# Optimization experiments

Hardware: AMD Instinct MI355X
Metric: run time of the kernel (lower is better)

## Reference

```python
import math
import jax, jax.numpy as jnp
import numpy as np

W_BITS = 8
A_BITS = 8
N_HEADS = 16

def fake_quant(x, bits):
    # symmetric per-tensor fake quantization with straight-through estimator
    if bits >= 32:
        return x
    qmax = float(2 ** (bits - 1) - 1)
    scale = jnp.maximum(jnp.max(jnp.abs(x)) / qmax, 1e-8)
    q = jnp.round(x / scale) * scale
    return x + jax.lax.stop_gradient(q - x)

def qlinear(x, W, b):
    # QuantizeLinear: quantize activations (a_bits) and weights (w_bits), then y = x @ W^T + b
    xq = fake_quant(x, A_BITS)
    Wq = fake_quant(W, W_BITS)
    return jnp.einsum('bsd,ed->bse', xq, Wq) + b

def setup_inputs() -> dict:
    key = jax.random.key(0)
    B, S, D = 2, 2048, 1024
    ks = jax.random.split(key, 6)
    inp = {
        'hidden_states': jax.random.normal(ks[0], (B, S, D), dtype=jnp.float32),
        'attention_mask': jnp.ones((B, S), dtype=jnp.float32),
        'Wq': 0.02 * jax.random.normal(ks[1], (D, D), dtype=jnp.float32),
        'bq': jnp.zeros((D,), dtype=jnp.float32),
        'Wk': 0.02 * jax.random.normal(ks[2], (D, D), dtype=jnp.float32),
        'bk': jnp.zeros((D,), dtype=jnp.float32),
        'Wv': 0.02 * jax.random.normal(ks[3], (D, D), dtype=jnp.float32),
        'bv': jnp.zeros((D,), dtype=jnp.float32),
        'Wo': 0.02 * jax.random.normal(ks[4], (D, D), dtype=jnp.float32),
        'bo': jnp.zeros((D,), dtype=jnp.float32),
    }
    return inp

def reference(hidden_states, attention_mask, Wq, bq, Wk, bk, Wv, bv, Wo, bo):
    B, S, D = hidden_states.shape
    H = N_HEADS
    hd = D // H

    q = qlinear(hidden_states, Wq, bq).reshape(B, S, H, hd)
    k = qlinear(hidden_states, Wk, bk).reshape(B, S, H, hd)
    v = qlinear(hidden_states, Wv, bv).reshape(B, S, H, hd)

    # scores: [B, H, Sq, Sk]
    scores = jnp.einsum('bqhd,bkhd->bhqk', q, k) / math.sqrt(hd)
    mask_bias = (1.0 - attention_mask)[:, None, None, :] * -10000.0
    scores = scores + mask_bias
    probs = jax.nn.softmax(scores, axis=-1)

    attn = jnp.einsum('bhqk,bkhd->bqhd', probs, v).reshape(B, S, D)
    return qlinear(attn, Wo, bo)
```

## Files before the change

kernel.cpp:

```cpp
#include <hip/hip_runtime.h>
#include <cstddef>
#include <cstdint>

constexpr int Bb = 2, Ss = 2048, Dd = 1024, Hh = 16, HD = 64;
constexpr int Mm = Bb * Ss;

typedef int v4i __attribute__((ext_vector_type(4)));
typedef __bf16 bf16x8 __attribute__((ext_vector_type(8)));
typedef __bf16 bf16x2 __attribute__((ext_vector_type(2)));
typedef float f32x16 __attribute__((ext_vector_type(16)));

#define QPOSTMUL 0.18033688f
#define MASKBIAS -14426.950408f

__device__ __forceinline__ float qscale(float amax) {
    return fmaxf(amax / 127.0f, 1e-8f);
}

__device__ __forceinline__ unsigned short bf16rtn(float x) {
    __bf16 b = (__bf16)x;
    return __builtin_bit_cast(unsigned short, b);
}

__device__ __forceinline__ unsigned pack_bf16x2(float a, float b) {
    bf16x2 h;
    h[0] = (__bf16)a;
    h[1] = (__bf16)b;
    return __builtin_bit_cast(unsigned, h);
}

__global__ void amax_all(const float4* __restrict__ hidden,
                         const float4* __restrict__ w0, const float4* __restrict__ w1,
                         const float4* __restrict__ w2, const float4* __restrict__ w3,
                         unsigned* __restrict__ slots) {
    const float4* src; int n4, slot, bx, nb;
    if (blockIdx.x < 448) { src = hidden; n4 = Mm * Dd / 4; slot = 0; bx = blockIdx.x; nb = 448; }
    else {
        int w = (blockIdx.x - 448) >> 4; bx = (blockIdx.x - 448) & 15; nb = 16;
        src = w == 0 ? w0 : w == 1 ? w1 : w == 2 ? w2 : w3;
        n4 = Dd * Dd / 4; slot = 1 + w;
    }
    float m = 0.f;
    for (int i = bx * blockDim.x + threadIdx.x; i < n4; i += nb * blockDim.x) {
        float4 v = src[i];
        m = fmaxf(m, fmaxf(fmaxf(fabsf(v.x), fabsf(v.y)), fmaxf(fabsf(v.z), fabsf(v.w))));
    }
    #pragma unroll
    for (int off = 32; off > 0; off >>= 1) m = fmaxf(m, __shfl_down(m, off, 64));
    __shared__ float sm[4];
    int lane = threadIdx.x & 63, wid = threadIdx.x >> 6;
    if (lane == 0) sm[wid] = m;
    __syncthreads();
    if (threadIdx.x == 0) {
        float mm = fmaxf(fmaxf(sm[0], sm[1]), fmaxf(sm[2], sm[3]));
        atomicMax(slots + slot, __float_as_uint(mm));
    }
}

__global__ void quant_all(const float* __restrict__ hidden,
                          const float* __restrict__ w0, const float* __restrict__ w1,
                          const float* __restrict__ w2, const float* __restrict__ w3,
                          const float* __restrict__ amax,
                          char* __restrict__ hq8, char* __restrict__ Wall8) {
    const float* x; char* y; int n4, slot, bx, nb;
    if (blockIdx.x < 1024) { x = hidden; y = hq8; n4 = Mm * Dd / 4; slot = 0; bx = blockIdx.x; nb = 1024; }
    else {
        int w = (blockIdx.x - 1024) >> 5; bx = (blockIdx.x - 1024) & 31; nb = 32;
        x = w == 0 ? w0 : w == 1 ? w1 : w == 2 ? w2 : w3;
        y = Wall8 + ((size_t)w << 20);
        n4 = Dd * Dd / 4; slot = 1 + w;
    }
    float s = qscale(amax[slot]);
    const float4* x4 = (const float4*)x;
    char4* y4 = (char4*)y;
    for (int i = bx * blockDim.x + threadIdx.x; i < n4; i += nb * blockDim.x) {
        float4 v = x4[i];
        char4 q;
        q.x = (char)(int)rintf(v.x / s);
        q.y = (char)(int)rintf(v.y / s);
        q.z = (char)(int)rintf(v.z / s);
        q.w = (char)(int)rintf(v.w / s);
        y4[i] = q;
    }
}

__global__ void quant_a(const float* __restrict__ x, char* __restrict__ y,
                        const float* __restrict__ amax, int n4) {
    float s = qscale(amax[0]);
    int stride = gridDim.x * blockDim.x;
    const float4* x4 = (const float4*)x;
    char4* y4 = (char4*)y;
    for (int i = blockIdx.x * blockDim.x + threadIdx.x; i < n4; i += stride) {
        float4 v = x4[i];
        char4 q;
        q.x = (char)(int)rintf(v.x / s);
        q.y = (char)(int)rintf(v.y / s);
        q.z = (char)(int)rintf(v.z / s);
        q.w = (char)(int)rintf(v.w / s);
        y4[i] = q;
    }
}

#define GLOAD_LDS16(g, l) __builtin_amdgcn_global_load_lds( \
    (const __attribute__((address_space(1))) unsigned int*)(g), \
    (__attribute__((address_space(3))) unsigned int*)(l), 16, 0, 0)

__device__ __forceinline__ void gemm128_core(const char* __restrict__ A, const char* __restrict__ Bw,
                                             int bm, int bn, int K, int t,
                                             char* At, char* Bt, v4i acc[4][4]) {
    const int lane = t & 63, w = t >> 6;
    const int wm = (w >> 1) * 64, wn = (w & 1) * 64;
    const int lr = lane & 15, kq = lane >> 4;
    const int rs = w * 16 + (lane >> 2);
    const int cc = lane & 3;

    for (int k0 = 0; k0 < K; k0 += 64) {
        __syncthreads();
        #pragma unroll
        for (int h = 0; h < 2; h++) {
            int r = rs + h * 64;
            int cs = cc ^ ((r >> 1) & 3);
            GLOAD_LDS16(A  + (size_t)(bm + r) * K + k0 + cs * 16, At + r * 64 + cc * 16);
            GLOAD_LDS16(Bw + (size_t)(bn + r) * K + k0 + cs * 16, Bt + r * 64 + cc * 16);
        }
        __syncthreads();

        v4i af[4], bf[4];
        #pragma unroll
        for (int mt = 0; mt < 4; mt++) {
            int row = wm + mt * 16 + lr;
            af[mt] = *(const v4i*)(At + row * 64 + ((kq ^ ((row >> 1) & 3)) << 4));
        }
        #pragma unroll
        for (int nt = 0; nt < 4; nt++) {
            int row = wn + nt * 16 + lr;
            bf[nt] = *(const v4i*)(Bt + row * 64 + ((kq ^ ((row >> 1) & 3)) << 4));
        }
        #pragma unroll
        for (int mt = 0; mt < 4; mt++)
            #pragma unroll
            for (int nt = 0; nt < 4; nt++)
                acc[mt][nt] = __builtin_amdgcn_mfma_i32_16x16x64_i8(af[mt], bf[nt], acc[mt][nt], 0, 0, 0);
    }
}

__global__ __launch_bounds__(256) void gemm_qkv(const char* __restrict__ A,
                                                const char* __restrict__ Wall8,
                                                const float* __restrict__ bq,
                                                const float* __restrict__ bk,
                                                const float* __restrict__ bv,
                                                const float* __restrict__ amax,
                                                unsigned short* __restrict__ qb16,
                                                unsigned short* __restrict__ kb16,
                                                unsigned short* __restrict__ vt16) {
    __shared__ alignas(16) char pool[34816];
    char* At = pool;
    char* Bt = pool + 8192;
    unsigned short (*Tt)[136] = (unsigned short(*)[136])pool;

    const int t = threadIdx.x, lane = t & 63, w = t >> 6;
    const int mat = blockIdx.x >> 3;
    const int bn = (blockIdx.x & 7) * 128, bm = blockIdx.y * 128;
    const int wm = (w >> 1) * 64, wn = (w & 1) * 64;
    const int lr = lane & 15, kq = lane >> 4;

    const v4i vzero = {0, 0, 0, 0};
    v4i acc[4][4];
    #pragma unroll
    for (int mt = 0; mt < 4; mt++)
        #pragma unroll
        for (int nt = 0; nt < 4; nt++) acc[mt][nt] = vzero;

    const char* Bw = Wall8 + ((size_t)mat << 20);
    gemm128_core(A, Bw, bm, bn, Dd, t, At, Bt, acc);

    const float* bias = mat == 0 ? bq : mat == 1 ? bk : bv;
    float sc = qscale(amax[0]) * qscale(amax[1 + mat]);
    float pm = (mat == 0) ? QPOSTMUL : 1.0f;

    __syncthreads();

    if (mat != 2) {
        #pragma unroll
        for (int nt = 0; nt < 4; nt++) {
            int n_l = wn + nt * 16 + lr;
            float bv_ = bias[bn + n_l];
            #pragma unroll
            for (int mt = 0; mt < 4; mt++) {
                int m_l = wm + mt * 16 + kq * 4;
                #pragma unroll
                for (int rg = 0; rg < 4; rg++)
                    Tt[m_l + rg][n_l] = bf16rtn(((float)acc[mt][nt][rg] * sc + bv_) * pm);
            }
        }
    } else {
        #pragma unroll
        for (int nt = 0; nt < 4; nt++) {
            int n_l = wn + nt * 16 + lr;
            float bv_ = bias[bn + n_l];
            #pragma unroll
            for (int mt = 0; mt < 4; mt++) {
                int m_l = wm + mt * 16 + kq * 4;
                ushort4 hv;
                hv.x = bf16rtn((float)acc[mt][nt][0] * sc + bv_);
                hv.y = bf16rtn((float)acc[mt][nt][1] * sc + bv_);
                hv.z = bf16rtn((float)acc[mt][nt][2] * sc + bv_);
                hv.w = bf16rtn((float)acc[mt][nt][3] * sc + bv_);
                *(ushort4*)&Tt[n_l][m_l] = hv;
            }
        }
    }
    __syncthreads();

    {
        int row = t >> 1, half = t & 1;
        unsigned short* dst;
        if (mat != 2) {
            dst = (mat == 0 ? qb16 : kb16) + (size_t)(bm + row) * Dd + bn + half * 64;
        } else {
            int n = bn + row;
            int e = n & 63, hc = n >> 6;
            int b_ = bm >> 11, s_ = (bm & 2047) + half * 64;
            dst = vt16 + (((size_t)(b_ * Hh + hc) * 64 + e) * Ss) + s_;
        }
        const unsigned short* srcl = &Tt[row][half * 64];
        #pragma unroll
        for (int c = 0; c < 8; c++)
            *(int4*)(dst + c * 8) = *(const int4*)(srcl + c * 8);
    }
}

__global__ __launch_bounds__(256) void gemm_o(const char* __restrict__ A,
                                              const char* __restrict__ Bw,
                                              const float* __restrict__ bias,
                                              const float* __restrict__ amaxA,
                                              const float* __restrict__ amaxB,
                                              float* __restrict__ C) {
    __shared__ alignas(16) char At[128 * 64];
    __shared__ alignas(16) char Bt[64 * 64];
    const int t = threadIdx.x, lane = t & 63, w = t >> 6;
    const int bn = blockIdx.x * 64, bm = blockIdx.y * 128;
    const int wm = (w >> 1) * 64, wn = (w & 1) * 32;
    const int lr = lane & 15, kq = lane >> 4;
    const int rs = t >> 2, cc = t & 3;
    const int cs = cc ^ ((rs >> 1) & 3);
    const int rs2 = rs + 64, cs2 = cc ^ ((rs2 >> 1) & 3);

    const v4i vzero = {0, 0, 0, 0};
    v4i acc[4][2];
    #pragma unroll
    for (int mt = 0; mt < 4; mt++) { acc[mt][0] = vzero; acc[mt][1] = vzero; }

    for (int k0 = 0; k0 < Dd; k0 += 64) {
        __syncthreads();
        GLOAD_LDS16(A  + (size_t)(bm + rs)  * Dd + k0 + cs  * 16, At + rs  * 64 + cc * 16);
        GLOAD_LDS16(A  + (size_t)(bm + rs2) * Dd + k0 + cs2 * 16, At + rs2 * 64 + cc * 16);
        GLOAD_LDS16(Bw + (size_t)(bn + rs)  * Dd + k0 + cs  * 16, Bt + rs  * 64 + cc * 16);
        __syncthreads();

        v4i af[4], bf[2];
        #pragma unroll
        for (int mt = 0; mt < 4; mt++) {
            int row = wm + mt * 16 + lr;
            af[mt] = *(const v4i*)(At + row * 64 + ((kq ^ ((row >> 1) & 3)) << 4));
        }
        #pragma unroll
        for (int nt = 0; nt < 2; nt++) {
            int row = wn + nt * 16 + lr;
            bf[nt] = *(const v4i*)(Bt + row * 64 + ((kq ^ ((row >> 1) & 3)) << 4));
        }
        #pragma unroll
        for (int mt = 0; mt < 4; mt++)
            #pragma unroll
            for (int nt = 0; nt < 2; nt++)
                acc[mt][nt] = __builtin_amdgcn_mfma_i32_16x16x64_i8(af[mt], bf[nt], acc[mt][nt], 0, 0, 0);
    }

    float sc = qscale(amaxA[0]) * qscale(amaxB[0]);
    #pragma unroll
    for (int nt = 0; nt < 2; nt++) {
        int n = bn + wn + nt * 16 + lr;
        float bv_ = bias[n];
        #pragma unroll
        for (int mt = 0; mt < 4; mt++)
            #pragma unroll
            for (int rg = 0; rg < 4; rg++) {
                int m = bm + wm + mt * 16 + kq * 4 + rg;
                C[(size_t)m * Dd + n] = (float)acc[mt][nt][rg] * sc + bv_;
            }
    }
}

__global__ __launch_bounds__(512) void attn_mfma(
    const unsigned short* __restrict__ qb16, const unsigned short* __restrict__ kb16,
    const unsigned short* __restrict__ vt16,
    const float* __restrict__ mask, float* __restrict__ Ob, unsigned* __restrict__ amax_out) {
    __shared__ alignas(16) char apool[36864];
    unsigned short (*Ks)[64][72] = (unsigned short(*)[64][72])apool;
    unsigned short (*Vs)[64][72] = (unsigned short(*)[64][72])(apool + 18432);
    __shared__ alignas(16) unsigned PwU[8][32][36];
    __shared__ float mbias[2][64];
    __shared__ float wred[4];

    const int t = threadIdx.x, lane = t & 63, wq = t >> 6;
    const int g = wq >> 2, wq4 = wq & 3, tg = t & 255;
    const int ln31 = lane & 31, h5 = lane >> 5;
    const int b = blockIdx.z, h = blockIdx.y, q0 = blockIdx.x * 128;
    const int kbase = g << 10;

    bf16x8 qf[4];
    {
        int qrow = q0 + wq4 * 32 + ln31;
        const unsigned short* qb_ = qb16 + ((size_t)(b * Ss + qrow)) * Dd + h * 64 + h5 * 8;
        #pragma unroll
        for (int c = 0; c < 4; c++) qf[c] = *(const bf16x8*)(qb_ + c * 16);
    }

    const int srow = tg >> 2, cp = (tg & 3) * 2;
    const int rho = (srow >> 1) + (srow & 1) * 32;
    int4 pk0, pk1, pv0, pv1; float pmask = 1.f;
    auto prefetch = [&](int k0) {
        const unsigned short* gk = kb16 + ((size_t)(b * Ss + k0 + srow)) * Dd + h * 64 + cp * 8;
        const unsigned short* gv = vt16 + (((size_t)(b * Hh + h) * 64 + srow)) * Ss + k0 + cp * 8;
        pk0 = *(const int4*)gk; pk1 = *(const int4*)(gk + 8);
        pv0 = *(const int4*)gv; pv1 = *(const int4*)(gv + 8);
        if (tg < 64) pmask = mask[b * Ss + k0 + tg];
    };

    f32x16 o0 = 0.f, o1 = 0.f;
    float lp[16];
    #pragma unroll
    for (int r = 0; r < 16; r++) lp[r] = 0.f;

    prefetch(kbase);
    for (int k0 = kbase; k0 < kbase + Ss / 2; k0 += 64) {
        __syncthreads();
        *(int4*)&Ks[g][rho][cp * 8]      = pk0;
        *(int4*)&Ks[g][rho][cp * 8 + 8]  = pk1;
        *(int4*)&Vs[g][srow][cp * 8]     = pv0;
        *(int4*)&Vs[g][srow][cp * 8 + 8] = pv1;
        if (tg < 64) mbias[g][tg] = (1.0f - pmask) * MASKBIAS;
        __syncthreads();
        if (k0 + 64 < kbase + Ss / 2) prefetch(k0 + 64);

        f32x16 sc0 = 0.f, sc1 = 0.f;
        __builtin_amdgcn_s_setprio(1);
        #pragma unroll
        for (int c = 0; c < 4; c++) {
            bf16x8 kh0 = *(const bf16x8*)&Ks[g][ln31][c * 16 + h5 * 8];
            bf16x8 kh1 = *(const bf16x8*)&Ks[g][32 + ln31][c * 16 + h5 * 8];
            sc0 = __builtin_amdgcn_mfma_f32_32x32x16_bf16(qf[c], kh0, sc0, 0, 0, 0);
            sc1 = __builtin_amdgcn_mfma_f32_32x32x16_bf16(qf[c], kh1, sc1, 0, 0, 0);
        }
        __builtin_amdgcn_s_setprio(0);

        float mb0 = mbias[g][2 * ln31], mb1 = mbias[g][2 * ln31 + 1];
        #pragma unroll
        for (int r = 0; r < 16; r++) {
            float p0 = __builtin_amdgcn_exp2f(sc0[r] + mb0);
            float p1 = __builtin_amdgcn_exp2f(sc1[r] + mb1);
            lp[r] += p0 + p1;
            int row = (r & 3) + 8 * (r >> 2) + 4 * h5;
            PwU[wq][row][ln31] = pack_bf16x2(p0, p1);
        }

        __builtin_amdgcn_s_setprio(1);
        #pragma unroll
        for (int c = 0; c < 4; c++) {
            bf16x8 pf = *(const bf16x8*)((const unsigned short*)&PwU[wq][ln31][0] + c * 16 + h5 * 8);
            bf16x8 vh0 = *(const bf16x8*)&Vs[g][ln31][c * 16 + h5 * 8];
            bf16x8 vh1 = *(const bf16x8*)&Vs[g][32 + ln31][c * 16 + h5 * 8];
            o0 = __builtin_amdgcn_mfma_f32_32x32x16_bf16(pf, vh0, o0, 0, 0, 0);
            o1 = __builtin_amdgcn_mfma_f32_32x32x16_bf16(pf, vh1, o1, 0, 0, 0);
        }
        __builtin_amdgcn_s_setprio(0);
    }

    __syncthreads();
    float (*Osh)[65] = (float(*)[65])apool;
    float* Lsh = (float*)(apool + 33280);

    if (g == 1) {
        #pragma unroll
        for (int r = 0; r < 16; r++) {
            float l = lp[r];
            #pragma unroll
            for (int off = 1; off < 32; off <<= 1) l += __shfl_xor(l, off, 32);
            int rl = wq4 * 32 + (r & 3) + 8 * (r >> 2) + 4 * h5;
            Osh[rl][ln31]      = o0[r];
            Osh[rl][32 + ln31] = o1[r];
            if (ln31 == 0) Lsh[rl] = l;
        }
    }
    __syncthreads();
    if (g == 0) {
        float lmax = 0.f;
        #pragma unroll
        for (int r = 0; r < 16; r++) {
            float l = lp[r];
            #pragma unroll
            for (int off = 1; off < 32; off <<= 1) l += __shfl_xor(l, off, 32);
            int rl = wq4 * 32 + (r & 3) + 8 * (r >> 2) + 4 * h5;
            float inv = 1.0f / (l + Lsh[rl]);
            int row = q0 + rl;
            size_t ro = ((size_t)(b * Ss + row)) * Dd + h * 64;
            float v0 = (o0[r] + Osh[rl][ln31]) * inv;
            float v1 = (o1[r] + Osh[rl][32 + ln31]) * inv;
            Ob[ro + ln31]      = v0;
            Ob[ro + 32 + ln31] = v1;
            lmax = fmaxf(lmax, fmaxf(fabsf(v0), fabsf(v1)));
        }
        #pragma unroll
        for (int off = 32; off > 0; off >>= 1) lmax = fmaxf(lmax, __shfl_xor(lmax, off, 64));
        if (lane == 0) wred[wq4] = lmax;
    }
    __syncthreads();
    if (t == 0) {
        float m = fmaxf(fmaxf(wred[0], wred[1]), fmaxf(wred[2], wred[3]));
        atomicMax(amax_out, __float_as_uint(m));
    }
}

extern "C" void kernel_launch(void* const* d_in, const int* in_sizes, int n_in,
                              void* d_out, int out_size, void* d_ws, size_t ws_size,
                              hipStream_t stream) {
    const float* hidden = (const float*)d_in[0];
    const float* mask   = (const float*)d_in[1];
    const float* Wq = (const float*)d_in[2];
    const float* bq = (const float*)d_in[3];
    const float* Wk = (const float*)d_in[4];
    const float* bk = (const float*)d_in[5];
    const float* Wv = (const float*)d_in[6];
    const float* bv = (const float*)d_in[7];
    const float* Wo = (const float*)d_in[8];
    const float* bo = (const float*)d_in[9];
    float* out = (float*)d_out;

    char* ws = (char*)d_ws;
    float* scal = (float*)ws;
    size_t off = 1024;
    const size_t szH8 = (size_t)Mm * Dd;
    const size_t szHb = (size_t)Mm * Dd * sizeof(unsigned short);
    const size_t szHf = (size_t)Mm * Dd * sizeof(float);
    char* hq8   = ws + off; off += szH8;
    char* Wall8 = ws + off; off += 4u << 20;
    char* aq8   = ws + off; off += szH8;
    unsigned short* qb16 = (unsigned short*)(ws + off); off += szHb;
    unsigned short* kb16 = (unsigned short*)(ws + off); off += szHb;
    unsigned short* vt16 = (unsigned short*)(ws + off); off += szHb;
    float* ab = (float*)(ws + off); off += szHf;

    hipMemsetAsync(scal, 0, 64, stream);

    amax_all<<<512, 256, 0, stream>>>((const float4*)hidden, (const float4*)Wq,
                                      (const float4*)Wk, (const float4*)Wv, (const float4*)Wo,
                                      (unsigned*)scal);
    quant_all<<<1152, 256, 0, stream>>>(hidden, Wq, Wk, Wv, Wo, scal, hq8, Wall8);

    gemm_qkv<<<dim3(24, 32), 256, 0, stream>>>(hq8, Wall8, bq, bk, bv, scal,
                                               qb16, kb16, vt16);

    attn_mfma<<<dim3(Ss / 128, Hh, Bb), 512, 0, stream>>>(qb16, kb16, vt16,
                                                          mask, ab, (unsigned*)(scal + 5));

    quant_a<<<1024, 256, 0, stream>>>(ab, aq8, scal + 5, Mm * Dd / 4);

    gemm_o<<<dim3(16, 32), 256, 0, stream>>>(aq8, Wall8 + (3u << 20), bo,
                                             scal + 5, scal + 4, out);
}
```

Measured before the change: 232.5 us.

## Compute transposed scores so probabilities feed PV MFMA directly from registers

Swaps the MFMA operand order for QK^T so each lane holds scores in the layout needed as the A operand of the PV MFMA. This removes the LDS round trip for the probability tile and the per-row shuffle reductions of the row sums. The mask becomes a wave ballot bitmask that is applied only when some key is masked, and launch bounds ask for higher occupancy. The risks are register pressure from the occupancy hint and correctness of the reworked fragment layout and mask semantics; non-binary mask values are now thresholded at 0.5.

Result: faster. 218.9 us (-5.9%).

```diff
diff --git a/kernel.cpp b/kernel.cpp
--- a/kernel.cpp
+++ b/kernel.cpp
@@ -11,7 +11,6 @@
 typedef float f32x16 __attribute__((ext_vector_type(16)));
 
 #define QPOSTMUL 0.18033688f
-#define MASKBIAS -14426.950408f
 
 __device__ __forceinline__ float qscale(float amax) {
     return fmaxf(amax / 127.0f, 1e-8f);
@@ -291,15 +290,13 @@
     }
 }
 
-__global__ __launch_bounds__(512) void attn_mfma(
+__global__ __launch_bounds__(512, 4) void attn_mfma(
     const unsigned short* __restrict__ qb16, const unsigned short* __restrict__ kb16,
     const unsigned short* __restrict__ vt16,
     const float* __restrict__ mask, float* __restrict__ Ob, unsigned* __restrict__ amax_out) {
     __shared__ alignas(16) char apool[36864];
     unsigned short (*Ks)[64][72] = (unsigned short(*)[64][72])apool;
     unsigned short (*Vs)[64][72] = (unsigned short(*)[64][72])(apool + 18432);
-    __shared__ alignas(16) unsigned PwU[8][32][36];
-    __shared__ float mbias[2][64];
     __shared__ float wred[4];
 
     const int t = threadIdx.x, lane = t & 63, wq = t >> 6;
@@ -318,19 +315,17 @@
 
     const int srow = tg >> 2, cp = (tg & 3) * 2;
     const int rho = (srow >> 1) + (srow & 1) * 32;
-    int4 pk0, pk1, pv0, pv1; float pmask = 1.f;
+    int4 pk0, pk1, pv0, pv1; float pmv = 1.f;
     auto prefetch = [&](int k0) {
         const unsigned short* gk = kb16 + ((size_t)(b * Ss + k0 + srow)) * Dd + h * 64 + cp * 8;
         const unsigned short* gv = vt16 + (((size_t)(b * Hh + h) * 64 + srow)) * Ss + k0 + cp * 8;
         pk0 = *(const int4*)gk; pk1 = *(const int4*)(gk + 8);
         pv0 = *(const int4*)gv; pv1 = *(const int4*)(gv + 8);
-        if (tg < 64) pmask = mask[b * Ss + k0 + tg];
+        pmv = mask[b * Ss + k0 + lane];
     };
 
     f32x16 o0 = 0.f, o1 = 0.f;
-    float lp[16];
-    #pragma unroll
-    for (int r = 0; r < 16; r++) lp[r] = 0.f;
+    float la0 = 0.f, la1 = 0.f, la2 = 0.f, la3 = 0.f;
 
     prefetch(kbase);
     for (int k0 = kbase; k0 < kbase + Ss / 2; k0 += 64) {
@@ -339,7 +334,7 @@
         *(int4*)&Ks[g][rho][cp * 8 + 8]  = pk1;
         *(int4*)&Vs[g][srow][cp * 8]     = pv0;
         *(int4*)&Vs[g][srow][cp * 8 + 8] = pv1;
-        if (tg < 64) mbias[g][tg] = (1.0f - pmask) * MASKBIAS;
+        unsigned long long bm = __ballot(pmv > 0.5f);
         __syncthreads();
         if (k0 + 64 < kbase + Ss / 2) prefetch(k0 + 64);
 
@@ -349,47 +344,61 @@
         for (int c = 0; c < 4; c++) {
             bf16x8 kh0 = *(const bf16x8*)&Ks[g][ln31][c * 16 + h5 * 8];
             bf16x8 kh1 = *(const bf16x8*)&Ks[g][32 + ln31][c * 16 + h5 * 8];
-            sc0 = __builtin_amdgcn_mfma_f32_32x32x16_bf16(qf[c], kh0, sc0, 0, 0, 0);
-            sc1 = __builtin_amdgcn_mfma_f32_32x32x16_bf16(qf[c], kh1, sc1, 0, 0, 0);
+            sc0 = __builtin_amdgcn_mfma_f32_32x32x16_bf16(kh0, qf[c], sc0, 0, 0, 0);
+            sc1 = __builtin_amdgcn_mfma_f32_32x32x16_bf16(kh1, qf[c], sc1, 0, 0, 0);
         }
         __builtin_amdgcn_s_setprio(0);
 
-        float mb0 = mbias[g][2 * ln31], mb1 = mbias[g][2 * ln31 + 1];
-        #pragma unroll
-        for (int r = 0; r < 16; r++) {
-            float p0 = __builtin_amdgcn_exp2f(sc0[r] + mb0);
-            float p1 = __builtin_amdgcn_exp2f(sc1[r] + mb1);
-            lp[r] += p0 + p1;
-            int row = (r & 3) + 8 * (r >> 2) + 4 * h5;
-            PwU[wq][row][ln31] = pack_bf16x2(p0, p1);
-        }
-
-        __builtin_amdgcn_s_setprio(1);
         #pragma unroll
         for (int c = 0; c < 4; c++) {
-            bf16x8 pf = *(const bf16x8*)((const unsigned short*)&PwU[wq][ln31][0] + c * 16 + h5 * 8);
+            float e0[4], e1[4];
+            #pragma unroll
+            for (int j = 0; j < 4; j++) {
+                e0[j] = __builtin_amdgcn_exp2f(sc0[4 * c + j]);
+                e1[j] = __builtin_amdgcn_exp2f(sc1[4 * c + j]);
+            }
+            if (bm != ~0ull) {
+                #pragma unroll
+                for (int j = 0; j < 4; j++) {
+                    int kk = 16 * c + 8 * h5 + 2 * j;
+                    e0[j] *= (float)(int)((bm >> kk) & 1);
+                    e1[j] *= (float)(int)((bm >> (kk + 1)) & 1);
+                }
+            }
+            la0 += e0[0] + e1[0];
+            la1 += e0[1] + e1[1];
+            la2 += e0[2] + e1[2];
+            la3 += e0[3] + e1[3];
+
+            uint4 pw;
+            pw.x = pack_bf16x2(e0[0], e1[0]);
+            pw.y = pack_bf16x2(e0[1], e1[1]);
+            pw.z = pack_bf16x2(e0[2], e1[2]);
+            pw.w = pack_bf16x2(e0[3], e1[3]);
+            bf16x8 pf = __builtin_bit_cast(bf16x8, pw);
             bf16x8 vh0 = *(const bf16x8*)&Vs[g][ln31][c * 16 + h5 * 8];
             bf16x8 vh1 = *(const bf16x8*)&Vs[g][32 + ln31][c * 16 + h5 * 8];
+            __builtin_amdgcn_s_setprio(1);
             o0 = __builtin_amdgcn_mfma_f32_32x32x16_bf16(pf, vh0, o0, 0, 0, 0);
             o1 = __builtin_amdgcn_mfma_f32_32x32x16_bf16(pf, vh1, o1, 0, 0, 0);
-        }
-        __builtin_amdgcn_s_setprio(0);
-    }
+            __builtin_amdgcn_s_setprio(0);
+        }
+    }
+
+    float lsum = (la0 + la1) + (la2 + la3);
+    lsum += __shfl_xor(lsum, 32, 64);
 
     __syncthreads();
     float (*Osh)[65] = (float(*)[65])apool;
-    float* Lsh = (float*)(apool + 33280);
-
+    float (*Lsh2)[128] = (float(*)[128])(apool + 33280);
+
+    if (lane < 32) Lsh2[g][wq4 * 32 + ln31] = lsum;
     if (g == 1) {
         #pragma unroll
         for (int r = 0; r < 16; r++) {
-            float l = lp[r];
-            #pragma unroll
-            for (int off = 1; off < 32; off <<= 1) l += __shfl_xor(l, off, 32);
             int rl = wq4 * 32 + (r & 3) + 8 * (r >> 2) + 4 * h5;
             Osh[rl][ln31]      = o0[r];
             Osh[rl][32 + ln31] = o1[r];
-            if (ln31 == 0) Lsh[rl] = l;
         }
     }
     __syncthreads();
@@ -397,13 +406,9 @@
         float lmax = 0.f;
         #pragma unroll
         for (int r = 0; r < 16; r++) {
-            float l = lp[r];
-            #pragma unroll
-            for (int off = 1; off < 32; off <<= 1) l += __shfl_xor(l, off, 32);
             int rl = wq4 * 32 + (r & 3) + 8 * (r >> 2) + 4 * h5;
-            float inv = 1.0f / (l + Lsh[rl]);
-            int row = q0 + rl;
-            size_t ro = ((size_t)(b * Ss + row)) * Dd + h * 64;
+            float inv = 1.0f / (Lsh2[0][rl] + Lsh2[1][rl]);
+            size_t ro = ((size_t)(b * Ss + q0 + rl)) * Dd + h * 64;
             float v0 = (o0[r] + Osh[rl][ln31]) * inv;
             float v1 = (o1[r] + Osh[rl][32 + ln31]) * inv;
             Ob[ro + ln31]      = v0;
```
